# Kernel tuning notes

Measured on AMD Instinct MI355X. Metric: run time of the kernel, lower is better.

The kernel has to match this reference:

```python
import jax, jax.numpy as jnp
import numpy as np

BITS = 4
GROUPSIZE = 128
MAXQ = 2 ** BITS - 1
PACK = 32 // BITS  # values packed per int32


def setup_inputs() -> dict:
    key = jax.random.key(0)
    k1, k2, k3, k4 = jax.random.split(key, 4)
    infeatures, outfeatures = 4096, 11008
    G = infeatures // GROUPSIZE  # 32 quantization groups
    x = jax.random.normal(k1, (16, 1, infeatures), dtype=jnp.float32)
    qweight = jax.random.randint(k2, (infeatures // PACK, outfeatures), 0, 2147483647, dtype=jnp.int32)
    scales = jax.random.uniform(k3, (G, outfeatures), dtype=jnp.float32)
    qzeros = jax.random.randint(k4, (G, outfeatures // PACK), 0, 2147483647, dtype=jnp.int32)
    return {"x": x, "qweight": qweight, "scales": scales, "qzeros": qzeros}


def _dequant(qweight, scales, qzeros):
    # shift amounts 0,4,8,...,28
    wf = jnp.arange(0, 32, BITS, dtype=jnp.int32)
    # unpack zero-points: [G, out/PACK, PACK] -> [G, 1, out]
    zeros = jnp.bitwise_and(jnp.right_shift(qzeros[:, :, None], wf[None, None, :]), MAXQ)
    zeros = zeros.reshape(zeros.shape[0], 1, -1).astype(scales.dtype)
    # unpack weights: [in/PACK, PACK, out] -> [G, GROUPSIZE, out]
    w = jnp.bitwise_and(jnp.right_shift(qweight[:, None, :], wf[None, :, None]), MAXQ)
    w = w.reshape(-1, GROUPSIZE, w.shape[-1]).astype(scales.dtype)
    sc = scales[:, None, :]  # [G, 1, out]
    weight = sc * w - sc * zeros  # per-group dequant
    return weight.reshape(-1, weight.shape[-1])  # [in, out]


def reference(x, qweight, scales, qzeros):
    W = _dequant(qweight, scales, qzeros)
    return jnp.matmul(x, W)  # [B, S, out]
```

## Files before the change

kernel.cpp:

```cpp
#include <hip/hip_runtime.h>


#define M_DIM 16
#define K_DIM 4096
#define N_DIM 11008
#define GS 128
#define KSPLIT 16
#define KC (K_DIM / KSPLIT)
#define GPC (KC / GS)
#define BLOCKN 128
#define NTHREADS 512

typedef __attribute__((ext_vector_type(8))) short short8;
typedef __attribute__((ext_vector_type(4))) float f32x4;

__device__ __forceinline__ float bfl(unsigned w) {
    union { unsigned u; float f; } c; c.u = w << 16; return c.f;
}
__device__ __forceinline__ float bfh(unsigned w) {
    union { unsigned u; float f; } c; c.u = w & 0xFFFF0000u; return c.f;
}

__global__ __launch_bounds__(NTHREADS) void qlin_fused(
    const float* __restrict__ x,
    const int*   __restrict__ qweight,
    const float* __restrict__ scales,
    const int*   __restrict__ qzeros,
    float*       __restrict__ outp,
    int nchunks)
{
    __shared__ __align__(16) unsigned short xs[M_DIM * KC];
    __shared__ __align__(16) float Xl[GPC * 16];

    const int tid  = threadIdx.x;
    const int lane = tid & 63, wave = tid >> 6;
    const int lmod = lane & 15, lhi = lane >> 4;
    const int n    = blockIdx.x * BLOCKN + wave * 16 + lmod;
    const int swzA = (lmod & 7) << 4;

    f32x4 outacc = {0.f, 0.f, 0.f, 0.f};

    for (int c = 0; c < nchunks; ++c) {
        const int ky0 = (blockIdx.y * nchunks + c) * KC;
        const int G0 = ky0 / GS, rowbase = ky0 >> 3;

        float    sg[GPC]; unsigned zg[GPC]; unsigned qw[GPC][4];
#pragma unroll
        for (int g = 0; g < GPC; ++g) {
            sg[g] = scales[(size_t)(G0 + g) * N_DIM + n];
            zg[g] = (unsigned)qzeros[(size_t)(G0 + g) * (N_DIM / 8) + (n >> 3)];
#pragma unroll
            for (int t = 0; t < 4; ++t)
                qw[g][t] = (unsigned)
                    qweight[(size_t)(rowbase + g * 16 + t * 4 + lhi) * N_DIM + n];
        }

        __syncthreads();
        {
            const int m  = tid >> 5;
            const int cc = tid & 31;
            const float4* xp =
                (const float4*)(x + (size_t)m * K_DIM + ky0 + cc * 8);
            const float4 v0 = xp[0], v1 = xp[1];
            union { short8 s; unsigned u[4]; } pk;
            asm("v_cvt_pk_bf16_f32 %0, %1, %2" : "=v"(pk.u[0]) : "v"(v0.x), "v"(v1.x));
            asm("v_cvt_pk_bf16_f32 %0, %1, %2" : "=v"(pk.u[1]) : "v"(v0.y), "v"(v1.y));
            asm("v_cvt_pk_bf16_f32 %0, %1, %2" : "=v"(pk.u[2]) : "v"(v0.z), "v"(v1.z));
            asm("v_cvt_pk_bf16_f32 %0, %1, %2" : "=v"(pk.u[3]) : "v"(v0.w), "v"(v1.w));
            const int byte = ((m * KC + cc * 8) * 2) ^ ((m & 7) << 4);
            *(short8*)((char*)xs + byte) = pk.s;
        }
        __syncthreads();

        if (wave < GPC) {
            const int g = wave;
            float xv = 0.f;
#pragma unroll
            for (int q = 0; q < 4; ++q) {
                const int byte =
                    ((lmod * KC + g * GS + lhi * 32 + q * 8) * 2) ^ swzA;
                union { short8 s; unsigned u[4]; } a;
                a.s = *(const short8*)((const char*)xs + byte);
#pragma unroll
                for (int p = 0; p < 4; ++p) xv += bfl(a.u[p]) + bfh(a.u[p]);
            }
            xv += __shfl_xor(xv, 16, 64);
            xv += __shfl_xor(xv, 32, 64);
            if (lane < 16) Xl[g * 16 + lane] = xv;
        }
        __syncthreads();

#pragma unroll
        for (int g = 0; g < GPC; ++g) {
            f32x4 acc = {0.f, 0.f, 0.f, 0.f};
#pragma unroll
            for (int t = 0; t < 4; ++t) {
                union { short8 v; unsigned u[4]; } b;
                const unsigned q = qw[g][t];
                b.u[0] = ( q        & 0x000F000Fu) | 0x43804380u;
                b.u[1] = ((q >> 4)  & 0x000F000Fu) | 0x43804380u;
                b.u[2] = ((q >> 8)  & 0x000F000Fu) | 0x43804380u;
                b.u[3] = ((q >> 12) & 0x000F000Fu) | 0x43804380u;
                const int byte =
                    ((lmod * KC + g * GS + t * 32 + lhi * 8) * 2) ^ swzA;
                const short8 a = *(const short8*)((const char*)xs + byte);
                acc = __builtin_amdgcn_mfma_f32_16x16x32_bf16(a, b.v, acc, 0, 0, 0);
            }
            const f32x4 x4 = *(const f32x4*)&Xl[g * 16 + lhi * 4];
            const float z  = (float)((zg[g] >> ((n & 7) * 4)) & 15u);
            const float s2 = 0.5f * sg[g];
            const float zc = -sg[g] * (128.0f + z);
#pragma unroll
            for (int r = 0; r < 4; ++r)
                outacc[r] = fmaf(s2, acc[r], fmaf(zc, x4[r], outacc[r]));
        }
    }

#pragma unroll
    for (int r = 0; r < 4; ++r)
        outp[(size_t)(blockIdx.y * M_DIM + lhi * 4 + r) * N_DIM + n] = outacc[r];
}

__global__ __launch_bounds__(256) void qlin_reduce(
    const float* __restrict__ part, float* __restrict__ out)
{
    const int i = blockIdx.x * 256 + threadIdx.x;
    if (i < M_DIM * N_DIM) {
        float s = 0.f;
#pragma unroll
        for (int c = 0; c < KSPLIT; ++c)
            s += part[(size_t)c * M_DIM * N_DIM + i];
        out[i] = s;
    }
}

extern "C" void kernel_launch(void* const* d_in, const int* in_sizes, int n_in,
                              void* d_out, int out_size, void* d_ws, size_t ws_size,
                              hipStream_t stream) {
    const float* x       = (const float*)d_in[0];
    const int*   qweight = (const int*)d_in[1];
    const float* scales  = (const float*)d_in[2];
    const int*   qzeros  = (const int*)d_in[3];
    float*       out     = (float*)d_out;

    const size_t part_bytes = (size_t)KSPLIT * M_DIM * N_DIM * sizeof(float);
    if (ws_size >= part_bytes) {
        float* part = (float*)d_ws;
        dim3 grid(N_DIM / BLOCKN, KSPLIT);
        qlin_fused<<<grid, NTHREADS, 0, stream>>>(x, qweight, scales, qzeros,
                                                  part, 1);
        qlin_reduce<<<(M_DIM * N_DIM + 255) / 256, 256, 0, stream>>>(part, out);
    } else {
        dim3 grid(N_DIM / BLOCKN, 1);
        qlin_fused<<<grid, NTHREADS, 0, stream>>>(x, qweight, scales, qzeros,
                                                  out, KSPLIT);
    }
}
```

Baseline: 17.47 us.

## Halve KSPLIT and block width, fuse x-sum into staging, double-buffer weight loads

Changes the split to KSPLIT=8 with 64-column, 256-thread blocks and adds an occupancy hint. The per-group x row sums are now computed while x is converted to bf16, using 16-lane shuffles, which removes one barrier and a second LDS read pass. Quantized weights are loaded one group ahead instead of all up front, which lowers register pressure. The trade-off is less memory-level parallelism from fewer outstanding loads, and each block now handles twice as many groups, which may expose load latency.

```diff
diff --git a/kernel.cpp b/kernel.cpp
--- a/kernel.cpp
+++ b/kernel.cpp
@@ -5,11 +5,11 @@
 #define K_DIM 4096
 #define N_DIM 11008
 #define GS 128
-#define KSPLIT 16
+#define KSPLIT 8
 #define KC (K_DIM / KSPLIT)
 #define GPC (KC / GS)
-#define BLOCKN 128
-#define NTHREADS 512
+#define BLOCKN 64
+#define NTHREADS 256
 
 typedef __attribute__((ext_vector_type(8))) short short8;
 typedef __attribute__((ext_vector_type(4))) float f32x4;
@@ -21,7 +21,7 @@
     union { unsigned u; float f; } c; c.u = w & 0xFFFF0000u; return c.f;
 }
 
-__global__ __launch_bounds__(NTHREADS) void qlin_fused(
+__global__ __launch_bounds__(NTHREADS, 8) void qlin_fused(
     const float* __restrict__ x,
     const int*   __restrict__ qweight,
     const float* __restrict__ scales,
@@ -37,6 +37,7 @@
     const int lmod = lane & 15, lhi = lane >> 4;
     const int n    = blockIdx.x * BLOCKN + wave * 16 + lmod;
     const int swzA = (lmod & 7) << 4;
+    const int zsh  = (n & 7) * 4;
 
     f32x4 outacc = {0.f, 0.f, 0.f, 0.f};
 
@@ -44,59 +45,74 @@
         const int ky0 = (blockIdx.y * nchunks + c) * KC;
         const int G0 = ky0 / GS, rowbase = ky0 >> 3;
 
-        float    sg[GPC]; unsigned zg[GPC]; unsigned qw[GPC][4];
+        __syncthreads();
+
+        const float* xb = x + ky0 + (size_t)lane * 8;
+        float Xp[4];
+#pragma unroll
+        for (int h = 0; h < 2; ++h) {
+            float4 v0[2], v1[2];
+#pragma unroll
+            for (int i = 0; i < 2; ++i) {
+                const float4* xp =
+                    (const float4*)(xb + (size_t)((h * 2 + i) * 4 + wave) * K_DIM);
+                v0[i] = xp[0]; v1[i] = xp[1];
+            }
+#pragma unroll
+            for (int i = 0; i < 2; ++i) {
+                const int m = (h * 2 + i) * 4 + wave;
+                union { short8 s; unsigned u[4]; } pk;
+                asm("v_cvt_pk_bf16_f32 %0, %1, %2" : "=v"(pk.u[0]) : "v"(v0[i].x), "v"(v1[i].x));
+                asm("v_cvt_pk_bf16_f32 %0, %1, %2" : "=v"(pk.u[1]) : "v"(v0[i].y), "v"(v1[i].y));
+                asm("v_cvt_pk_bf16_f32 %0, %1, %2" : "=v"(pk.u[2]) : "v"(v0[i].z), "v"(v1[i].z));
+                asm("v_cvt_pk_bf16_f32 %0, %1, %2" : "=v"(pk.u[3]) : "v"(v0[i].w), "v"(v1[i].w));
+                const int byte = ((m * KC + lane * 8) * 2) ^ ((m & 7) << 4);
+                *(short8*)((char*)xs + byte) = pk.s;
+                float s = 0.f;
+#pragma unroll
+                for (int p = 0; p < 4; ++p) s += bfl(pk.u[p]) + bfh(pk.u[p]);
+                Xp[h * 2 + i] = s;
+            }
+        }
+
+        float sg[GPC]; unsigned zg[GPC];
 #pragma unroll
         for (int g = 0; g < GPC; ++g) {
             sg[g] = scales[(size_t)(G0 + g) * N_DIM + n];
             zg[g] = (unsigned)qzeros[(size_t)(G0 + g) * (N_DIM / 8) + (n >> 3)];
+        }
+        unsigned qwc[4], qwn[4];
 #pragma unroll
-            for (int t = 0; t < 4; ++t)
-                qw[g][t] = (unsigned)
-                    qweight[(size_t)(rowbase + g * 16 + t * 4 + lhi) * N_DIM + n];
+        for (int t = 0; t < 4; ++t)
+            qwc[t] = (unsigned)qweight[(size_t)(rowbase + t * 4 + lhi) * N_DIM + n];
+
+#pragma unroll
+        for (int i = 0; i < 4; ++i) {
+            Xp[i] += __shfl_xor(Xp[i], 1, 16);
+            Xp[i] += __shfl_xor(Xp[i], 2, 16);
+            Xp[i] += __shfl_xor(Xp[i], 4, 16);
+            Xp[i] += __shfl_xor(Xp[i], 8, 16);
         }
-
-        __syncthreads();
-        {
-            const int m  = tid >> 5;
-            const int cc = tid & 31;
-            const float4* xp =
-                (const float4*)(x + (size_t)m * K_DIM + ky0 + cc * 8);
-            const float4 v0 = xp[0], v1 = xp[1];
-            union { short8 s; unsigned u[4]; } pk;
-            asm("v_cvt_pk_bf16_f32 %0, %1, %2" : "=v"(pk.u[0]) : "v"(v0.x), "v"(v1.x));
-            asm("v_cvt_pk_bf16_f32 %0, %1, %2" : "=v"(pk.u[1]) : "v"(v0.y), "v"(v1.y));
-            asm("v_cvt_pk_bf16_f32 %0, %1, %2" : "=v"(pk.u[2]) : "v"(v0.z), "v"(v1.z));
-            asm("v_cvt_pk_bf16_f32 %0, %1, %2" : "=v"(pk.u[3]) : "v"(v0.w), "v"(v1.w));
-            const int byte = ((m * KC + cc * 8) * 2) ^ ((m & 7) << 4);
-            *(short8*)((char*)xs + byte) = pk.s;
-        }
-        __syncthreads();
-
-        if (wave < GPC) {
-            const int g = wave;
-            float xv = 0.f;
+        if ((lane & 15) == 0) {
 #pragma unroll
-            for (int q = 0; q < 4; ++q) {
-                const int byte =
-                    ((lmod * KC + g * GS + lhi * 32 + q * 8) * 2) ^ swzA;
-                union { short8 s; unsigned u[4]; } a;
-                a.s = *(const short8*)((const char*)xs + byte);
-#pragma unroll
-                for (int p = 0; p < 4; ++p) xv += bfl(a.u[p]) + bfh(a.u[p]);
-            }
-            xv += __shfl_xor(xv, 16, 64);
-            xv += __shfl_xor(xv, 32, 64);
-            if (lane < 16) Xl[g * 16 + lane] = xv;
+            for (int i = 0; i < 4; ++i)
+                Xl[lhi * 16 + i * 4 + wave] = Xp[i];
         }
         __syncthreads();
 
 #pragma unroll
         for (int g = 0; g < GPC; ++g) {
+            if (g + 1 < GPC) {
+#pragma unroll
+                for (int t = 0; t < 4; ++t)
+                    qwn[t] = (unsigned)
+                        qweight[(size_t)(rowbase + (g + 1) * 16 + t * 4 + lhi) * N_DIM + n];
+            }
             f32x4 acc = {0.f, 0.f, 0.f, 0.f};
 #pragma unroll
             for (int t = 0; t < 4; ++t) {
                 union { short8 v; unsigned u[4]; } b;
-                const unsigned q = qw[g][t];
+                const unsigned q = qwc[t];
                 b.u[0] = ( q        & 0x000F000Fu) | 0x43804380u;
                 b.u[1] = ((q >> 4)  & 0x000F000Fu) | 0x43804380u;
                 b.u[2] = ((q >> 8)  & 0x000F000Fu) | 0x43804380u;
@@ -106,8 +122,11 @@
                 const short8 a = *(const short8*)((const char*)xs + byte);
                 acc = __builtin_amdgcn_mfma_f32_16x16x32_bf16(a, b.v, acc, 0, 0, 0);
             }
+#pragma unroll
+            for (int t = 0; t < 4; ++t) qwc[t] = qwn[t];
+
             const f32x4 x4 = *(const f32x4*)&Xl[g * 16 + lhi * 4];
-            const float z  = (float)((zg[g] >> ((n & 7) * 4)) & 15u);
+            const float z  = (float)((zg[g] >> zsh) & 15u);
             const float s2 = 0.5f * sg[g];
             const float zc = -sg[g] * (128.0f + z);
 #pragma unroll
```

Measured after the change: 23.72 us. +35.7%, slower.

## Replace split-K partial buffer and reduce kernel with atomic accumulation

Applied to the files above, without the earlier changes.

Drops the per-split partial-sum workspace and the separate reduction kernel. Output is now zeroed with a memset and each block atomically adds its partial results into it. The split-K factor goes from 16 to 4, blocks shrink to 64 columns with 256 threads, and each block preloads a larger x slice into shared memory. This removes a kernel launch and the partial-buffer traffic, at the cost of atomics, non-deterministic summation order, and more per-block work with fewer blocks in flight.

```diff
diff --git a/kernel.cpp b/kernel.cpp
--- a/kernel.cpp
+++ b/kernel.cpp
@@ -5,11 +5,11 @@
 #define K_DIM 4096
 #define N_DIM 11008
 #define GS 128
-#define KSPLIT 16
+#define KSPLIT 4
 #define KC (K_DIM / KSPLIT)
 #define GPC (KC / GS)
-#define BLOCKN 128
-#define NTHREADS 512
+#define BLOCKN 64
+#define NTHREADS 256
 
 typedef __attribute__((ext_vector_type(8))) short short8;
 typedef __attribute__((ext_vector_type(4))) float f32x4;
@@ -26,8 +26,7 @@
     const int*   __restrict__ qweight,
     const float* __restrict__ scales,
     const int*   __restrict__ qzeros,
-    float*       __restrict__ outp,
-    int nchunks)
+    float*       __restrict__ out)
 {
     __shared__ __align__(16) unsigned short xs[M_DIM * KC];
     __shared__ __align__(16) float Xl[GPC * 16];
@@ -37,101 +36,80 @@
     const int lmod = lane & 15, lhi = lane >> 4;
     const int n    = blockIdx.x * BLOCKN + wave * 16 + lmod;
     const int swzA = (lmod & 7) << 4;
+    const int zsh  = (n & 7) * 4;
+
+    const int ky0 = blockIdx.y * KC;
+    const int G0 = ky0 / GS, rowbase = ky0 >> 3;
+
+#pragma unroll
+    for (int i = 0; i < (M_DIM * KC / 8) / NTHREADS; ++i) {
+        const int idx = i * NTHREADS + tid;
+        const int m  = idx >> 7;
+        const int cc = idx & 127;
+        const float4* xp =
+            (const float4*)(x + (size_t)m * K_DIM + ky0 + cc * 8);
+        const float4 v0 = xp[0], v1 = xp[1];
+        union { short8 s; unsigned u[4]; } pk;
+        asm("v_cvt_pk_bf16_f32 %0, %1, %2" : "=v"(pk.u[0]) : "v"(v0.x), "v"(v1.x));
+        asm("v_cvt_pk_bf16_f32 %0, %1, %2" : "=v"(pk.u[1]) : "v"(v0.y), "v"(v1.y));
+        asm("v_cvt_pk_bf16_f32 %0, %1, %2" : "=v"(pk.u[2]) : "v"(v0.z), "v"(v1.z));
+        asm("v_cvt_pk_bf16_f32 %0, %1, %2" : "=v"(pk.u[3]) : "v"(v0.w), "v"(v1.w));
+        const int byte = ((m * KC + cc * 8) * 2) ^ ((m & 7) << 4);
+        *(short8*)((char*)xs + byte) = pk.s;
+    }
+    __syncthreads();
+
+#pragma unroll
+    for (int gg = wave; gg < GPC; gg += 4) {
+        float xv = 0.f;
+#pragma unroll
+        for (int q = 0; q < 4; ++q) {
+            const int byte =
+                ((lmod * KC + gg * GS + lhi * 32 + q * 8) * 2) ^ swzA;
+            union { short8 s; unsigned u[4]; } a;
+            a.s = *(const short8*)((const char*)xs + byte);
+#pragma unroll
+            for (int p = 0; p < 4; ++p) xv += bfl(a.u[p]) + bfh(a.u[p]);
+        }
+        xv += __shfl_xor(xv, 16, 64);
+        xv += __shfl_xor(xv, 32, 64);
+        if (lane < 16) Xl[gg * 16 + lane] = xv;
+    }
+    __syncthreads();
 
     f32x4 outacc = {0.f, 0.f, 0.f, 0.f};
-
-    for (int c = 0; c < nchunks; ++c) {
-        const int ky0 = (blockIdx.y * nchunks + c) * KC;
-        const int G0 = ky0 / GS, rowbase = ky0 >> 3;
-
-        float    sg[GPC]; unsigned zg[GPC]; unsigned qw[GPC][4];
 #pragma unroll
-        for (int g = 0; g < GPC; ++g) {
-            sg[g] = scales[(size_t)(G0 + g) * N_DIM + n];
-            zg[g] = (unsigned)qzeros[(size_t)(G0 + g) * (N_DIM / 8) + (n >> 3)];
+    for (int g = 0; g < GPC; ++g) {
+        const float s = scales[(size_t)(G0 + g) * N_DIM + n];
+        const unsigned zq =
+            (unsigned)qzeros[(size_t)(G0 + g) * (N_DIM / 8) + (n >> 3)];
+        f32x4 acc = {0.f, 0.f, 0.f, 0.f};
 #pragma unroll
-            for (int t = 0; t < 4; ++t)
-                qw[g][t] = (unsigned)
-                    qweight[(size_t)(rowbase + g * 16 + t * 4 + lhi) * N_DIM + n];
+        for (int t = 0; t < 4; ++t) {
+            const unsigned q = (unsigned)
+                qweight[(size_t)(rowbase + g * 16 + t * 4 + lhi) * N_DIM + n];
+            union { short8 v; unsigned u[4]; } b;
+            b.u[0] = ( q        & 0x000F000Fu) | 0x43804380u;
+            b.u[1] = ((q >> 4)  & 0x000F000Fu) | 0x43804380u;
+            b.u[2] = ((q >> 8)  & 0x000F000Fu) | 0x43804380u;
+            b.u[3] = ((q >> 12) & 0x000F000Fu) | 0x43804380u;
+            const int byte =
+                ((lmod * KC + g * GS + t * 32 + lhi * 8) * 2) ^ swzA;
+            const short8 a = *(const short8*)((const char*)xs + byte);
+            acc = __builtin_amdgcn_mfma_f32_16x16x32_bf16(a, b.v, acc, 0, 0, 0);
         }
-
-        __syncthreads();
-        {
-            const int m  = tid >> 5;
-            const int cc = tid & 31;
-            const float4* xp =
-                (const float4*)(x + (size_t)m * K_DIM + ky0 + cc * 8);
-            const float4 v0 = xp[0], v1 = xp[1];
-            union { short8 s; unsigned u[4]; } pk;
-            asm("v_cvt_pk_bf16_f32 %0, %1, %2" : "=v"(pk.u[0]) : "v"(v0.x), "v"(v1.x));
-            asm("v_cvt_pk_bf16_f32 %0, %1, %2" : "=v"(pk.u[1]) : "v"(v0.y), "v"(v1.y));
-            asm("v_cvt_pk_bf16_f32 %0, %1, %2" : "=v"(pk.u[2]) : "v"(v0.z), "v"(v1.z));
-            asm("v_cvt_pk_bf16_f32 %0, %1, %2" : "=v"(pk.u[3]) : "v"(v0.w), "v"(v1.w));
-            const int byte = ((m * KC + cc * 8) * 2) ^ ((m & 7) << 4);
-            *(short8*)((char*)xs + byte) = pk.s;
-        }
-        __syncthreads();
-
-        if (wave < GPC) {
-            const int g = wave;
-            float xv = 0.f;
+        const f32x4 x4 = *(const f32x4*)&Xl[g * 16 + lhi * 4];
+        const float z  = (float)((zq >> zsh) & 15u);
+        const float s2 = 0.5f * s;
+        const float zc = -s * (128.0f + z);
 #pragma unroll
-            for (int q = 0; q < 4; ++q) {
-                const int byte =
-                    ((lmod * KC + g * GS + lhi * 32 + q * 8) * 2) ^ swzA;
-                union { short8 s; unsigned u[4]; } a;
-                a.s = *(const short8*)((const char*)xs + byte);
-#pragma unroll
-                for (int p = 0; p < 4; ++p) xv += bfl(a.u[p]) + bfh(a.u[p]);
-            }
-            xv += __shfl_xor(xv, 16, 64);
-            xv += __shfl_xor(xv, 32, 64);
-            if (lane < 16) Xl[g * 16 + lane] = xv;
-        }
-        __syncthreads();
-
-#pragma unroll
-        for (int g = 0; g < GPC; ++g) {
-            f32x4 acc = {0.f, 0.f, 0.f, 0.f};
-#pragma unroll
-            for (int t = 0; t < 4; ++t) {
-                union { short8 v; unsigned u[4]; } b;
-                const unsigned q = qw[g][t];
-                b.u[0] = ( q        & 0x000F000Fu) | 0x43804380u;
-                b.u[1] = ((q >> 4)  & 0x000F000Fu) | 0x43804380u;
-                b.u[2] = ((q >> 8)  & 0x000F000Fu) | 0x43804380u;
-                b.u[3] = ((q >> 12) & 0x000F000Fu) | 0x43804380u;
-                const int byte =
-                    ((lmod * KC + g * GS + t * 32 + lhi * 8) * 2) ^ swzA;
-                const short8 a = *(const short8*)((const char*)xs + byte);
-                acc = __builtin_amdgcn_mfma_f32_16x16x32_bf16(a, b.v, acc, 0, 0, 0);
-            }
-            const f32x4 x4 = *(const f32x4*)&Xl[g * 16 + lhi * 4];
-            const float z  = (float)((zg[g] >> ((n & 7) * 4)) & 15u);
-            const float s2 = 0.5f * sg[g];
-            const float zc = -sg[g] * (128.0f + z);
-#pragma unroll
-            for (int r = 0; r < 4; ++r)
-                outacc[r] = fmaf(s2, acc[r], fmaf(zc, x4[r], outacc[r]));
-        }
+        for (int r = 0; r < 4; ++r)
+            outacc[r] = fmaf(s2, acc[r], fmaf(zc, x4[r], outacc[r]));
     }
 
 #pragma unroll
     for (int r = 0; r < 4; ++r)
-        outp[(size_t)(blockIdx.y * M_DIM + lhi * 4 + r) * N_DIM + n] = outacc[r];
-}
-
-__global__ __launch_bounds__(256) void qlin_reduce(
-    const float* __restrict__ part, float* __restrict__ out)
-{
-    const int i = blockIdx.x * 256 + threadIdx.x;
-    if (i < M_DIM * N_DIM) {
-        float s = 0.f;
-#pragma unroll
-        for (int c = 0; c < KSPLIT; ++c)
-            s += part[(size_t)c * M_DIM * N_DIM + i];
-        out[i] = s;
-    }
+        atomicAdd(&out[(size_t)(lhi * 4 + r) * N_DIM + n], outacc[r]);
 }
 
 extern "C" void kernel_launch(void* const* d_in, const int* in_sizes, int n_in,
@@ -143,16 +121,7 @@
     const int*   qzeros  = (const int*)d_in[3];
     float*       out     = (float*)d_out;
 
-    const size_t part_bytes = (size_t)KSPLIT * M_DIM * N_DIM * sizeof(float);
-    if (ws_size >= part_bytes) {
-        float* part = (float*)d_ws;
-        dim3 grid(N_DIM / BLOCKN, KSPLIT);
-        qlin_fused<<<grid, NTHREADS, 0, stream>>>(x, qweight, scales, qzeros,
-                                                  part, 1);
-        qlin_reduce<<<(M_DIM * N_DIM + 255) / 256, 256, 0, stream>>>(part, out);
-    } else {
-        dim3 grid(N_DIM / BLOCKN, 1);
-        qlin_fused<<<grid, NTHREADS, 0, stream>>>(x, qweight, scales, qzeros,
-                                                  out, KSPLIT);
-    }
+    hipMemsetAsync(out, 0, (size_t)out_size * sizeof(float), stream);
+    dim3 grid(N_DIM / BLOCKN, KSPLIT);
+    qlin_fused<<<grid, NTHREADS, 0, stream>>>(x, qweight, scales, qzeros, out);
 }
```

New measurement: 18.07 us. 1.03x slower.
